# Kernel tuning notes

Measured on AMD Instinct MI355X. Metric: run time of the kernel, lower is better.

Reference implementation:

```python
import jax, jax.numpy as jnp
import numpy as np

D = 256  # in_channels == out_channels -> output_proj is Identity


def setup_inputs() -> dict:
    key = jax.random.key(0)
    ks = jax.random.split(key, 7)
    B, N = 4, 4096
    s = 1.0 / np.sqrt(D)
    return {
        "x": jax.random.normal(ks[0], (B, N, D), dtype=jnp.float32),
        "Wk": jax.random.normal(ks[1], (D, D), dtype=jnp.float32) * s,
        "bk": jax.random.normal(ks[2], (D,), dtype=jnp.float32) * 0.01,
        "Wq": jax.random.normal(ks[3], (D, D), dtype=jnp.float32) * s,
        "bq": jax.random.normal(ks[4], (D,), dtype=jnp.float32) * 0.01,
        "Wv": jax.random.normal(ks[5], (D, D), dtype=jnp.float32) * s,
        "bv": jax.random.normal(ks[6], (D,), dtype=jnp.float32) * 0.01,
    }


def reference(x, Wk, bk, Wq, bq, Wv, bv):
    # Linear projections: torch Linear(x) = x @ W.T + b; here W is stored as [in, out]
    keys = jnp.einsum("bnd,de->bne", x, Wk) + bk
    queries = jnp.einsum("bnd,de->bne", x, Wq) + bq
    values = jnp.einsum("bnd,de->bne", x, Wv) + bv
    scale = 1.0 / jnp.sqrt(jnp.float32(D))
    scores = jnp.einsum("bqd,bkd->bqk", queries, keys) * scale  # [B, N, N]
    attn = jax.nn.softmax(scores, axis=-1)
    out = jnp.einsum("bqk,bkd->bqd", attn, values)
    return out
```

## Files before the change

### kernel.cpp

```cpp
#include <hip/hip_runtime.h>
#include <hip/hip_bf16.h>


typedef __attribute__((ext_vector_type(8))) short bf16x8;
typedef __attribute__((ext_vector_type(4))) float f32x4;
typedef __attribute__((ext_vector_type(4))) uint  u32x4;

__device__ __forceinline__ float b2f(ushort u){
  union { uint i; float f; } v; v.i = ((uint)u) << 16; return v.f;
}
__device__ __forceinline__ ushort f2b(float f){
  union { float f; uint i; } v; v.f = f;
  uint i = v.i;
  return (ushort)((i + 0x7FFFu + ((i >> 16) & 1u)) >> 16);
}
__device__ __forceinline__ uint pack2(float a, float b){
  return (uint)f2b(a) | ((uint)f2b(b) << 16);
}
__device__ __forceinline__ uint fbits(float f){
  union { float f; uint i; } v; v.f = f; return v.i;
}

__device__ __forceinline__ void gl_lds16(const ushort* g, ushort* l){
  __builtin_amdgcn_global_load_lds(
      (const __attribute__((address_space(1))) uint*)g,
      (__attribute__((address_space(3))) uint*)l, 16, 0, 0);
}

#define Q_SCALE 0.0901684400555602f
#define FIXED_M 16.0f

__global__ __launch_bounds__(256) void transpose_w_kernel(
    const float* __restrict__ Wk, const float* __restrict__ Wq,
    const float* __restrict__ Wv, ushort* __restrict__ Wt){
  __shared__ ushort t[64][72];
  const float* src = (blockIdx.y == 0) ? Wk : (blockIdx.y == 1) ? Wq : Wv;
  ushort* dst = Wt + blockIdx.y * 65536;
  int tile = blockIdx.x;
  int tr = tile >> 2, tc = tile & 3;
  int tid = threadIdx.x;
  for (int i = tid; i < 1024; i += 256){
    int r = i >> 4, ch = i & 15;
    float4 f = *(const float4*)(src + (tr*64 + r)*256 + tc*64 + ch*4);
    uint2 u; u.x = pack2(f.x, f.y); u.y = pack2(f.z, f.w);
    *(uint2*)&t[r][ch*4] = u;
  }
  __syncthreads();
  for (int i = tid; i < 2048; i += 256){
    int c = i >> 5, r2 = (i & 31)*2;
    uint v = (uint)t[r2][c] | ((uint)t[r2+1][c] << 16);
    *(uint*)(dst + (tc*64 + c)*256 + tr*64 + r2) = v;
  }
}

__global__ __launch_bounds__(256) void proj_kernel(
    const float* __restrict__ x, const ushort* __restrict__ Wt,
    const float* __restrict__ bK, const float* __restrict__ bQ,
    const float* __restrict__ bV,
    ushort* __restrict__ Ko, ushort* __restrict__ Qo, ushort* __restrict__ Vt){
  __shared__ ushort xs[64][264];
  __shared__ ushort wt[2][16][264];
  int my = blockIdx.y;
  int n0 = blockIdx.x * 64;
  const ushort* wsrc = Wt + my*65536;
  const float* bias  = (my==0) ? bK : (my==1) ? bQ : bV;

  int tid = threadIdx.x;
  int lane = tid & 63, w = tid >> 6, quad = lane >> 4, l16 = lane & 15;

  for (int i = tid; i < 4096; i += 256){
    int r = i >> 6, ch = i & 63;
    float4 f = *(const float4*)(x + (size_t)(n0 + r)*256 + ch*4);
    uint2 u; u.x = pack2(f.x, f.y); u.y = pack2(f.z, f.w);
    *(uint2*)&xs[r][ch*4] = u;
  }

  int seg0 = tid*2,     r0 = seg0 >> 5, c0 = seg0 & 31;
  int seg1 = tid*2 + 1, r1 = seg1 >> 5, c1 = seg1 & 31;
  {
    uint4 a = *(const uint4*)(wsrc + r0*256 + c0*8);
    uint4 b = *(const uint4*)(wsrc + r1*256 + c1*8);
    *(uint4*)&wt[0][r0][c0*8] = a;
    *(uint4*)&wt[0][r1][c1*8] = b;
  }
  __syncthreads();

  bf16x8 afr[8];
  #pragma unroll
  for (int ks = 0; ks < 8; ks++)
    afr[ks] = *(const bf16x8*)&xs[w*16 + l16][ks*32 + quad*8];

  for (int nt = 0; nt < 16; nt++){
    int cu = nt & 1;
    uint4 wa, wb;
    if (nt < 15){
      const ushort* wn = wsrc + (nt+1)*4096;
      wa = *(const uint4*)(wn + r0*256 + c0*8);
      wb = *(const uint4*)(wn + r1*256 + c1*8);
    }
    f32x4 acc = {0.f, 0.f, 0.f, 0.f};
    #pragma unroll
    for (int ks = 0; ks < 8; ks++){
      bf16x8 bfr = *(const bf16x8*)&wt[cu][l16][ks*32 + quad*8];
      acc = __builtin_amdgcn_mfma_f32_16x16x32_bf16(afr[ks], bfr, acc, 0, 0, 0);
    }
    int e = nt*16 + l16;
    float bv = bias[e];
    if (my == 2){
      int b  = n0 >> 12;
      int nl = (n0 & 4095) + w*16 + quad*4;
      ushort* vb = Vt + (size_t)b*1048576 + (size_t)e*4096 + nl;
      #pragma unroll
      for (int r = 0; r < 4; r++) vb[r] = f2b(acc[r] + bv);
    } else {
      float scale = (my==1) ? Q_SCALE : 1.0f;
      ushort* out = (my==0) ? Ko : Qo;
      #pragma unroll
      for (int r = 0; r < 4; r++){
        int row = n0 + w*16 + quad*4 + r;
        out[(size_t)row*256 + e] = f2b((acc[r] + bv) * scale);
      }
    }
    if (nt < 15){
      *(uint4*)&wt[cu^1][r0][c0*8] = wa;
      *(uint4*)&wt[cu^1][r1][c1*8] = wb;
    }
    __syncthreads();
  }
}

__global__ __launch_bounds__(256, 2) void attn_kernel(
    const ushort* __restrict__ Q, const ushort* __restrict__ K,
    const ushort* __restrict__ Vt,
    float* __restrict__ O0, ushort* __restrict__ Obf, float* __restrict__ lp){
  __shared__ ushort Kbuf[2][8192];
  __shared__ ushort Vbuf[2][8192];

  int bx   = blockIdx.x;
  int bh   = bx & 15;
  int b    = bh >> 2;
  int half = bh & 3;
  int qt   = bx >> 4;
  int tid = threadIdx.x, lane = tid & 63, w = tid >> 6;
  int quad = lane >> 4, l16 = lane & 15;

  const ushort* Qb = Q  + (size_t)(b*4096 + qt*128)*256;
  const ushort* Kb = K  + (size_t)b*4096*256;
  const ushort* Vb = Vt + (size_t)b*256*4096;

  int kOff[4], vOff[4];
  #pragma unroll
  for (int i = 0; i < 4; i++){
    int off16 = (w*4 + i)*64 + lane;
    int krow = off16 >> 5, ks_ = off16 & 31;
    int g    = ks_ ^ (krow & 7);
    kOff[i]  = krow*256 + g*8;
    int sr = off16 >> 3, sl = off16 & 7;
    int xv = sl ^ (sr & 7);
    int d  = sr*2 + ((xv >> 2) & 1), c = xv & 3;
    vOff[i] = d*4096 + c*8;
  }
  int m7 = l16 & 7;
  int kslot[8];
  #pragma unroll
  for (int ks = 0; ks < 8; ks++) kslot[ks] = ((ks*4 + quad) ^ m7) * 8;
  int vlane = (((l16 >> 1)*8) + (((l16 & 1)*4 + quad) ^ (l16 >> 1))) * 8;

  int adrA = ((((2*quad    ) & 3) * 16 + l16) * 4);
  int adrB = ((((2*quad + 1) & 3) * 16 + l16) * 4);

  bf16x8 qf[2][8];
  #pragma unroll
  for (int s = 0; s < 2; s++)
    #pragma unroll
    for (int ks = 0; ks < 8; ks++)
      qf[s][ks] = *(const bf16x8*)(Qb + (size_t)(w*32 + s*16 + l16)*256 + ks*32 + quad*8);

  f32x4 of[2][16];
  #pragma unroll
  for (int s = 0; s < 2; s++)
    #pragma unroll
    for (int dt = 0; dt < 16; dt++) of[s][dt] = (f32x4){0.f, 0.f, 0.f, 0.f};
  float l_i[2] = {0.f, 0.f};

  int kt0 = half * 32, kt1 = kt0 + 32;

  #pragma unroll
  for (int i = 0; i < 4; i++){
    gl_lds16(Kb + (size_t)kt0*8192 + kOff[i], &Kbuf[0][(w*4 + i)*512]);
    gl_lds16(Vb + (size_t)kt0*32   + vOff[i], &Vbuf[0][(w*4 + i)*512]);
  }
  __syncthreads();

  int cur = 0;
  for (int kt = kt0; kt < kt1; kt++){
    int nxt = cur ^ 1;
    if (kt + 1 < kt1){
      #pragma unroll
      for (int i = 0; i < 4; i++){
        gl_lds16(Kb + (size_t)(kt+1)*8192 + kOff[i], &Kbuf[nxt][(w*4 + i)*512]);
        gl_lds16(Vb + (size_t)(kt+1)*32   + vOff[i], &Vbuf[nxt][(w*4 + i)*512]);
      }
    }
    const ushort* Kc = &Kbuf[cur][0];
    const ushort* Vc = &Vbuf[cur][0];

    f32x4 sf[2][2];
    #pragma unroll
    for (int s = 0; s < 2; s++)
      #pragma unroll
      for (int nt = 0; nt < 2; nt++) sf[s][nt] = (f32x4){0.f, 0.f, 0.f, 0.f};
    __builtin_amdgcn_s_setprio(1);
    #pragma unroll
    for (int nt = 0; nt < 2; nt++){
      const ushort* Kr = Kc + nt*4096 + l16*256;
      #pragma unroll
      for (int ks = 0; ks < 8; ks++){
        bf16x8 bfr = *(const bf16x8*)(Kr + kslot[ks]);
        sf[0][nt] = __builtin_amdgcn_mfma_f32_16x16x32_bf16(bfr, qf[0][ks], sf[0][nt], 0,0,0);
        sf[1][nt] = __builtin_amdgcn_mfma_f32_16x16x32_bf16(bfr, qf[1][ks], sf[1][nt], 0,0,0);
      }
    }
    __builtin_amdgcn_s_setprio(0);

    auto mkpf = [&](const f32x4& s0, const f32x4& s1, float& lacc) -> bf16x8 {
      float p00 = exp2f(s0[0] - FIXED_M), p01 = exp2f(s0[1] - FIXED_M);
      float p02 = exp2f(s0[2] - FIXED_M), p03 = exp2f(s0[3] - FIXED_M);
      float p10 = exp2f(s1[0] - FIXED_M), p11 = exp2f(s1[1] - FIXED_M);
      float p12 = exp2f(s1[2] - FIXED_M), p13 = exp2f(s1[3] - FIXED_M);
      lacc += ((p00 + p01) + (p02 + p03)) + ((p10 + p11) + (p12 + p13));
      uint pk00 = __builtin_amdgcn_perm(fbits(p01) + 0x8000u, fbits(p00) + 0x8000u, 0x07060302u);
      uint pk01 = __builtin_amdgcn_perm(fbits(p03) + 0x8000u, fbits(p02) + 0x8000u, 0x07060302u);
      uint pk10 = __builtin_amdgcn_perm(fbits(p11) + 0x8000u, fbits(p10) + 0x8000u, 0x07060302u);
      uint pk11 = __builtin_amdgcn_perm(fbits(p13) + 0x8000u, fbits(p12) + 0x8000u, 0x07060302u);
      bool lo = quad < 2;
      uint d0l = (uint)__builtin_amdgcn_ds_bpermute(adrA, (int)pk00);
      uint d0h = (uint)__builtin_amdgcn_ds_bpermute(adrA, (int)pk10);
      uint D0 = lo ? d0l : d0h;
      uint d1l = (uint)__builtin_amdgcn_ds_bpermute(adrA, (int)pk01);
      uint d1h = (uint)__builtin_amdgcn_ds_bpermute(adrA, (int)pk11);
      uint D1 = lo ? d1l : d1h;
      uint d2l = (uint)__builtin_amdgcn_ds_bpermute(adrB, (int)pk00);
      uint d2h = (uint)__builtin_amdgcn_ds_bpermute(adrB, (int)pk10);
      uint D2 = lo ? d2l : d2h;
      uint d3l = (uint)__builtin_amdgcn_ds_bpermute(adrB, (int)pk01);
      uint d3h = (uint)__builtin_amdgcn_ds_bpermute(adrB, (int)pk11);
      uint D3 = lo ? d3l : d3h;
      union { u32x4 u; bf16x8 v; } cv;
      cv.u = (u32x4){D0, D1, D2, D3};
      return cv.v;
    };
    bf16x8 pf0 = mkpf(sf[0][0], sf[0][1], l_i[0]);
    bf16x8 pf1 = mkpf(sf[1][0], sf[1][1], l_i[1]);

    __builtin_amdgcn_s_setprio(1);
    #pragma unroll
    for (int dt = 0; dt < 16; dt++){
      bf16x8 vf = *(const bf16x8*)(Vc + dt*512 + vlane);
      of[0][dt] = __builtin_amdgcn_mfma_f32_16x16x32_bf16(pf0, vf, of[0][dt], 0, 0, 0);
      of[1][dt] = __builtin_amdgcn_mfma_f32_16x16x32_bf16(pf1, vf, of[1][dt], 0, 0, 0);
    }
    __builtin_amdgcn_s_setprio(0);

    __syncthreads();
    cur = nxt;
  }

  #pragma unroll
  for (int s = 0; s < 2; s++){
    float rs = l_i[s];
    rs += __shfl_xor(rs, 16);
    rs += __shfl_xor(rs, 32);
    l_i[s] = rs;
  }

  #pragma unroll
  for (int s = 0; s < 2; s++){
    int gq0 = b*4096 + qt*128 + w*32 + s*16 + quad*4;
    if (quad == 0)
      lp[(size_t)half*16384 + b*4096 + qt*128 + w*32 + s*16 + l16] = l_i[s];
    if (half == 0){
      #pragma unroll
      for (int dt = 0; dt < 16; dt++)
        #pragma unroll
        for (int r = 0; r < 4; r++)
          O0[(size_t)(gq0 + r)*256 + dt*16 + l16] = of[s][dt][r];
    } else {
      ushort* Oh = Obf + (size_t)(half - 1)*16384*256;
      #pragma unroll
      for (int dt = 0; dt < 16; dt++)
        #pragma unroll
        for (int r = 0; r < 4; r++)
          Oh[(size_t)(gq0 + r)*256 + dt*16 + l16] = f2b(of[s][dt][r]);
    }
  }
}

__global__ __launch_bounds__(256) void merge_kernel(
    float* __restrict__ O0, const ushort* __restrict__ Obf,
    const float* __restrict__ lp){
  int t   = blockIdx.x*256 + threadIdx.x;
  int row = t >> 5;
  int c   = (t & 31) * 8;
  float den = lp[row] + lp[16384 + row] + lp[2*16384 + row] + lp[3*16384 + row];
  float rden = 1.0f / den;
  size_t idx = (size_t)row*256 + c;
  float4 a0 = *(float4*)&O0[idx];
  float4 a1 = *(float4*)&O0[idx + 4];
  #pragma unroll
  for (int h = 1; h < 4; h++){
    union { u32x4 u; ushort s[8]; } oh;
    oh.u = *(const u32x4*)&Obf[(size_t)(h-1)*16384*256 + idx];
    a0.x += b2f(oh.s[0]); a0.y += b2f(oh.s[1]);
    a0.z += b2f(oh.s[2]); a0.w += b2f(oh.s[3]);
    a1.x += b2f(oh.s[4]); a1.y += b2f(oh.s[5]);
    a1.z += b2f(oh.s[6]); a1.w += b2f(oh.s[7]);
  }
  a0.x *= rden; a0.y *= rden; a0.z *= rden; a0.w *= rden;
  a1.x *= rden; a1.y *= rden; a1.z *= rden; a1.w *= rden;
  *(float4*)&O0[idx]     = a0;
  *(float4*)&O0[idx + 4] = a1;
}

extern "C" void kernel_launch(void* const* d_in, const int* in_sizes, int n_in,
                              void* d_out, int out_size, void* d_ws, size_t ws_size,
                              hipStream_t stream){
  const float* x  = (const float*)d_in[0];
  const float* Wk = (const float*)d_in[1];
  const float* bk = (const float*)d_in[2];
  const float* Wq = (const float*)d_in[3];
  const float* bq = (const float*)d_in[4];
  const float* Wv = (const float*)d_in[5];
  const float* bv = (const float*)d_in[6];

  char* ws = (char*)d_ws;
  ushort* Wt  = (ushort*)(ws);
  ushort* Qb  = (ushort*)(ws + (size_t)1*(1u<<20));
  ushort* Kb  = (ushort*)(ws + (size_t)10*(1u<<20));
  ushort* Vtb = (ushort*)(ws + (size_t)19*(1u<<20));
  ushort* Obf = (ushort*)(ws + (size_t)28*(1u<<20));
  float*  lp  = (float*)(ws + (size_t)54*(1u<<20));

  hipLaunchKernelGGL(transpose_w_kernel, dim3(16, 3), dim3(256), 0, stream,
                     Wk, Wq, Wv, Wt);
  hipLaunchKernelGGL(proj_kernel, dim3(256, 3), dim3(256), 0, stream,
                     x, Wt, bk, bq, bv, Kb, Qb, Vtb);
  hipLaunchKernelGGL(attn_kernel, dim3(512), dim3(256), 0, stream,
                     Qb, Kb, Vtb, (float*)d_out, Obf, lp);
  hipLaunchKernelGGL(merge_kernel, dim3(2048), dim3(256), 0, stream,
                     (float*)d_out, Obf, lp);
}
```

Baseline: 191.7 us.

## Fuse split-K merge into attention kernel via last-arriver atomic counter

Removes the separate merge kernel launch. Each attention block bumps a per-tile atomic counter after writing its partial output, and the fourth block to arrive for a query tile sums the partials, normalises by the summed denominators and writes the final output. Counters are zeroed inside the projection kernel. This saves a launch and re-reading the block's own partial. In exchange the last block does serialized tail work with scalar strided loads, and correctness depends on threadfence ordering.

After: 385.1 us. 2.01x slower.

```diff
diff --git a/kernel.cpp b/kernel.cpp
--- a/kernel.cpp
+++ b/kernel.cpp
@@ -57,7 +57,8 @@
     const float* __restrict__ x, const ushort* __restrict__ Wt,
     const float* __restrict__ bK, const float* __restrict__ bQ,
     const float* __restrict__ bV,
-    ushort* __restrict__ Ko, ushort* __restrict__ Qo, ushort* __restrict__ Vt){
+    ushort* __restrict__ Ko, ushort* __restrict__ Qo, ushort* __restrict__ Vt,
+    uint* __restrict__ cnt){
   __shared__ ushort xs[64][264];
   __shared__ ushort wt[2][16][264];
   int my = blockIdx.y;
@@ -66,6 +67,7 @@
   const float* bias  = (my==0) ? bK : (my==1) ? bQ : bV;
 
   int tid = threadIdx.x;
+  if (my == 0 && blockIdx.x == 0 && tid < 128) cnt[tid] = 0;
   int lane = tid & 63, w = tid >> 6, quad = lane >> 4, l16 = lane & 15;
 
   for (int i = tid; i < 4096; i += 256){
@@ -132,9 +134,11 @@
 __global__ __launch_bounds__(256, 2) void attn_kernel(
     const ushort* __restrict__ Q, const ushort* __restrict__ K,
     const ushort* __restrict__ Vt,
-    float* __restrict__ O0, ushort* __restrict__ Obf, float* __restrict__ lp){
+    float* __restrict__ O0, ushort* __restrict__ Obf, float* __restrict__ lp,
+    uint* __restrict__ cnt){
   __shared__ ushort Kbuf[2][8192];
   __shared__ ushort Vbuf[2][8192];
+  __shared__ int ordS;
 
   int bx   = blockIdx.x;
   int bh   = bx & 15;
@@ -294,32 +298,37 @@
           Oh[(size_t)(gq0 + r)*256 + dt*16 + l16] = f2b(of[s][dt][r]);
     }
   }
-}
-
-__global__ __launch_bounds__(256) void merge_kernel(
-    float* __restrict__ O0, const ushort* __restrict__ Obf,
-    const float* __restrict__ lp){
-  int t   = blockIdx.x*256 + threadIdx.x;
-  int row = t >> 5;
-  int c   = (t & 31) * 8;
-  float den = lp[row] + lp[16384 + row] + lp[2*16384 + row] + lp[3*16384 + row];
-  float rden = 1.0f / den;
-  size_t idx = (size_t)row*256 + c;
-  float4 a0 = *(float4*)&O0[idx];
-  float4 a1 = *(float4*)&O0[idx + 4];
-  #pragma unroll
-  for (int h = 1; h < 4; h++){
-    union { u32x4 u; ushort s[8]; } oh;
-    oh.u = *(const u32x4*)&Obf[(size_t)(h-1)*16384*256 + idx];
-    a0.x += b2f(oh.s[0]); a0.y += b2f(oh.s[1]);
-    a0.z += b2f(oh.s[2]); a0.w += b2f(oh.s[3]);
-    a1.x += b2f(oh.s[4]); a1.y += b2f(oh.s[5]);
-    a1.z += b2f(oh.s[6]); a1.w += b2f(oh.s[7]);
-  }
-  a0.x *= rden; a0.y *= rden; a0.z *= rden; a0.w *= rden;
-  a1.x *= rden; a1.y *= rden; a1.z *= rden; a1.w *= rden;
-  *(float4*)&O0[idx]     = a0;
-  *(float4*)&O0[idx + 4] = a1;
+
+  __threadfence();
+  __syncthreads();
+  if (tid == 0) ordS = (int)(atomicAdd(cnt + (qt*4 + b), 1u) & 3u);
+  __syncthreads();
+  if (ordS == 3){
+    __threadfence();
+    #pragma unroll
+    for (int s = 0; s < 2; s++){
+      int gq0 = b*4096 + qt*128 + w*32 + s*16 + quad*4;
+      float rden[4];
+      #pragma unroll
+      for (int r = 0; r < 4; r++){
+        int q = gq0 + r;
+        rden[r] = 1.0f / (lp[q] + lp[16384 + q] + lp[2*16384 + q] + lp[3*16384 + q]);
+      }
+      #pragma unroll
+      for (int dt = 0; dt < 16; dt++)
+        #pragma unroll
+        for (int r = 0; r < 4; r++){
+          size_t idx = (size_t)(gq0 + r)*256 + dt*16 + l16;
+          float v = of[s][dt][r];
+          if (half != 0) v += O0[idx];
+          #pragma unroll
+          for (int h = 1; h < 4; h++)
+            if (h != half)
+              v += b2f(Obf[(size_t)(h-1)*16384*256 + idx]);
+          O0[idx] = v * rden[r];
+        }
+    }
+  }
 }
 
 extern "C" void kernel_launch(void* const* d_in, const int* in_sizes, int n_in,
@@ -340,13 +349,12 @@
   ushort* Vtb = (ushort*)(ws + (size_t)19*(1u<<20));
   ushort* Obf = (ushort*)(ws + (size_t)28*(1u<<20));
   float*  lp  = (float*)(ws + (size_t)54*(1u<<20));
+  uint*   cnt = (uint*)(ws + (size_t)54*(1u<<20) + 262144);
 
   hipLaunchKernelGGL(transpose_w_kernel, dim3(16, 3), dim3(256), 0, stream,
                      Wk, Wq, Wv, Wt);
   hipLaunchKernelGGL(proj_kernel, dim3(256, 3), dim3(256), 0, stream,
-                     x, Wt, bk, bq, bv, Kb, Qb, Vtb);
+                     x, Wt, bk, bq, bv, Kb, Qb, Vtb, cnt);
   hipLaunchKernelGGL(attn_kernel, dim3(512), dim3(256), 0, stream,
-                     Qb, Kb, Vtb, (float*)d_out, Obf, lp);
-  hipLaunchKernelGGL(merge_kernel, dim3(2048), dim3(256), 0, stream,
-                     (float*)d_out, Obf, lp);
-}
+                     Qb, Kb, Vtb, (float*)d_out, Obf, lp, cnt);
+}
```
